# Kernel tuning notes

Hardware: AMD Instinct MI355X
Metric: run time of the kernel (lower is better)

The kernel has to match this reference:

```python
import jax, jax.numpy as jnp
import numpy as np

N = 50000      # nodes
E = 1600000    # edges
F_IN = 128     # input_dim
H = 160        # hidden_dim
G = 512        # graphs in batch
C = 2          # num_classes
EPS = 1e-5     # BatchNorm eps


def setup_inputs() -> dict:
    key = jax.random.key(0)
    ks = jax.random.split(key, 12)
    x = jax.random.normal(ks[0], (N, F_IN), jnp.float32)
    edge_index = jax.random.randint(ks[1], (2, E), 0, N, dtype=jnp.int32)
    batch = jnp.sort(jax.random.randint(ks[2], (N,), 0, G, dtype=jnp.int32))

    def lin(k, fi, fo):
        s = 1.0 / np.sqrt(fi)
        kw, kb = jax.random.split(k)
        W = jax.random.uniform(kw, (fi, fo), jnp.float32, -s, s)
        b = jax.random.uniform(kb, (fo,), jnp.float32, -s, s)
        return W, b

    W1, b1 = lin(ks[3], F_IN, H)
    W2, b2 = lin(ks[4], H, H)
    W3, b3 = lin(ks[5], H, H)
    Wc1, bc1 = lin(ks[6], H, H // 2)
    Wc2, bc2 = lin(ks[7], H // 2, C)

    def bn(k):
        k1, k2, k3, k4 = jax.random.split(k, 4)
        gamma = jax.random.uniform(k1, (H,), jnp.float32, 0.5, 1.5)
        beta = jax.random.normal(k2, (H,), jnp.float32) * 0.1
        mean = jax.random.normal(k3, (H,), jnp.float32) * 0.1
        var = jax.random.uniform(k4, (H,), jnp.float32, 0.5, 1.5)
        return gamma, beta, mean, var

    g1, be1, m1, v1 = bn(ks[8])
    g2, be2, m2, v2 = bn(ks[9])
    g3, be3, m3, v3 = bn(ks[10])

    return dict(x=x, edge_index=edge_index, batch=batch,
                W1=W1, b1=b1, W2=W2, b2=b2, W3=W3, b3=b3,
                g1=g1, be1=be1, m1=m1, v1=v1,
                g2=g2, be2=be2, m2=m2, v2=v2,
                g3=g3, be3=be3, m3=m3, v3=v3,
                Wc1=Wc1, bc1=bc1, Wc2=Wc2, bc2=bc2)


def gcn_conv(x, W, b, src, dst):
    """PyG GCNConv: symmetric deg normalization with self-loops; lin -> aggregate -> +bias."""
    n = x.shape[0]
    h = x @ W                                   # [N, H]
    loop = jnp.arange(n, dtype=src.dtype)
    s = jnp.concatenate([src, loop])            # self-loops appended
    d = jnp.concatenate([dst, loop])
    deg = jax.ops.segment_sum(jnp.ones_like(d, jnp.float32), d, num_segments=n)
    inv = jnp.where(deg > 0, jax.lax.rsqrt(deg), 0.0)
    msg = h[s] * (inv[s] * inv[d])[:, None]     # [E+N, H] gather + norm
    return jax.ops.segment_sum(msg, d, num_segments=n) + b


def bn_eval(x, gamma, beta, mean, var):
    return (x - mean) * jax.lax.rsqrt(var + EPS) * gamma + beta


def reference(x, edge_index, batch, W1, b1, W2, b2, W3, b3,
              g1, be1, m1, v1, g2, be2, m2, v2, g3, be3, m3, v3,
              Wc1, bc1, Wc2, bc2):
    src, dst = edge_index[0], edge_index[1]
    # eval mode: dropout is identity, BN uses running stats
    h = jax.nn.relu(bn_eval(gcn_conv(x, W1, b1, src, dst), g1, be1, m1, v1))
    h = jax.nn.relu(bn_eval(gcn_conv(h, W2, b2, src, dst), g2, be2, m2, v2))
    h = jax.nn.relu(bn_eval(gcn_conv(h, W3, b3, src, dst), g3, be3, m3, v3))
    # global mean pool over graph ids
    sums = jax.ops.segment_sum(h, batch, num_segments=G)
    cnt = jax.ops.segment_sum(jnp.ones((h.shape[0],), jnp.float32), batch, num_segments=G)
    pooled = sums / jnp.clip(cnt, 1.0)[:, None]
    # MLP head
    z = jax.nn.relu(pooled @ Wc1 + bc1)
    return z @ Wc2 + bc2
```

## Files before the change

kernel.cpp:

```cpp
#include <hip/hip_runtime.h>

#define N_NODES   50000
#define N_EDGES   1600000
#define FDIM_IN   128
#define HDIM      160
#define N_GRAPHS  512
#define BN_EPS    1e-5f
#define NBKT_MAX  256
#define BKT_SH    8
#define HIST_BLOCKS 128

typedef _Float16 h2   __attribute__((ext_vector_type(2)));
typedef _Float16 f16x8 __attribute__((ext_vector_type(8)));
typedef float  facc4 __attribute__((ext_vector_type(4)));


__device__ __forceinline__ unsigned short f2h_bits(float f) {
    union { _Float16 h; unsigned short s; } c;
    c.h = (_Float16)f;
    return c.s;
}

__device__ __forceinline__ unsigned int pkh(float lo, float hi) {
    return (unsigned int)f2h_bits(lo) | ((unsigned int)f2h_bits(hi) << 16);
}

__device__ __forceinline__ h2 u2h(unsigned int u) {
    union { unsigned int u; h2 h; } c; c.u = u; return c.h;
}

__device__ __forceinline__ unsigned int h2u(h2 h) {
    union { unsigned int u; h2 h; } c; c.h = h; return c.u;
}

__device__ __forceinline__ void addpk16(h2* acc, uint4 r) {
    acc[0] += u2h(r.x);
    acc[1] += u2h(r.y);
    acc[2] += u2h(r.z);
    acc[3] += u2h(r.w);
}


__global__ __launch_bounds__(256) void coarse_hist_kernel(const int* __restrict__ dst,
                                                          int* __restrict__ cg, int E) {
    __shared__ int h[NBKT_MAX];
    int tid = threadIdx.x;
    if (tid < NBKT_MAX) h[tid] = 0;
    __syncthreads();
    for (int e = blockIdx.x * 256 + tid; e < E; e += gridDim.x * 256)
        atomicAdd(&h[dst[e] >> BKT_SH], 1);
    __syncthreads();
    if (tid < NBKT_MAX) cg[blockIdx.x * NBKT_MAX + tid] = h[tid];
}


struct PrepArgs {
    const float *b, *g, *be, *m, *v;
    float *sc, *sh;
};

__global__ __launch_bounds__(256) void setup_kernel(const int* __restrict__ cg,
                                                    int* __restrict__ bucket_base,
                                                    int* __restrict__ bucket_cursor,
                                                    PrepArgs a0, PrepArgs a1, PrepArgs a2,
                                                    const float* __restrict__ W1,
                                                    const float* __restrict__ W2,
                                                    const float* __restrict__ W3,
                                                    unsigned short* __restrict__ o1,
                                                    unsigned short* __restrict__ o2,
                                                    unsigned short* __restrict__ o3) {
    int bid = blockIdx.x;
    int t = threadIdx.x;
    if (bid == 0) {
        __shared__ int h[NBKT_MAX];
        __shared__ int total;
        if (t < NBKT_MAX) {
            int s = 0;
            for (int b = 0; b < HIST_BLOCKS; ++b) s += cg[b * NBKT_MAX + t];
            h[t] = s;
        }
        __syncthreads();
        if (t == 0) {
            int run = 0;
            for (int i = 0; i < NBKT_MAX; ++i) { int c = h[i]; h[i] = run; run += c; }
            total = run;
        }
        __syncthreads();
        if (t < NBKT_MAX) {
            bucket_base[t] = h[t];
            bucket_cursor[t] = h[t];
        }
        if (t == 0) bucket_base[NBKT_MAX] = total;
    } else if (bid <= 3) {
        PrepArgs a = (bid == 1) ? a0 : (bid == 2) ? a1 : a2;
        if (t < HDIM) {
            float s = a.g[t] * rsqrtf(a.v[t] + BN_EPS);
            a.sc[t] = s;
            a.sh[t] = (a.b[t] - a.m[t]) * s + a.be[t];
        }
    } else {
        int i = (bid - 4) * 256 + t;
        const float* W;
        unsigned short* o;
        if (i < 128 * 160)                 { W = W1; o = o1; }
        else if (i < 128 * 160 + 160 * 160) { W = W2; o = o2; i -= 128 * 160; }
        else if (i < 128 * 160 + 2 * 160 * 160) { W = W3; o = o3; i -= 128 * 160 + 160 * 160; }
        else return;
        int j = i & 7;
        int l = (i >> 3) & 63;
        int u = (i >> 9) % 10;
        int tt = i / 5120;
        int k = tt * 32 + (l >> 4) * 8 + j;
        int nn = u * 16 + (l & 15);
        o[i] = f2h_bits(W[k * 160 + nn]);
    }
}

__global__ __launch_bounds__(256) void part_kernel(const int* __restrict__ src,
                                                   const int* __restrict__ dst,
                                                   int* __restrict__ bucket_cursor,
                                                   unsigned int* __restrict__ pairs, int E) {
    __shared__ int bcnt[NBKT_MAX], bbase[NBKT_MAX], lc[NBKT_MAX];
    int tid = threadIdx.x;
    int per = (E + gridDim.x - 1) / gridDim.x;
    int beg = blockIdx.x * per;
    int end = min(beg + per, E);
    if (tid < NBKT_MAX) { bcnt[tid] = 0; lc[tid] = 0; }
    __syncthreads();
    for (int e = beg + tid; e < end; e += 256)
        atomicAdd(&bcnt[dst[e] >> BKT_SH], 1);
    __syncthreads();
    if (tid < NBKT_MAX)
        bbase[tid] = bcnt[tid] ? atomicAdd(&bucket_cursor[tid], bcnt[tid]) : 0;
    __syncthreads();
    for (int e = beg + tid; e < end; e += 256) {
        int d = dst[e];
        int b = d >> BKT_SH;
        int pos = bbase[b] + atomicAdd(&lc[b], 1);
        pairs[pos] = ((unsigned int)src[e] << BKT_SH) | (unsigned int)(d & (NBKT_MAX - 1));
    }
}

__global__ __launch_bounds__(1024) void bucket_csr_kernel(const unsigned int* __restrict__ pairs,
                                                          const int* __restrict__ bucket_base,
                                                          int* __restrict__ row_off,
                                                          float* __restrict__ inv,
                                                          int* __restrict__ ssrc,
                                                          const float* __restrict__ x,
                                                          unsigned short* __restrict__ xs,
                                                          int n) {
    __shared__ int h[NBKT_MAX];
    __shared__ int ws[4];
    __shared__ float sinv[NBKT_MAX];
    int tid = threadIdx.x;
    int b = blockIdx.x;
    int node0 = b << BKT_SH;
    int beg = bucket_base[b], end = bucket_base[b + 1];
    if (tid < NBKT_MAX) h[tid] = 0;
    __syncthreads();
    for (int j = beg + tid; j < end; j += 1024)
        atomicAdd(&h[pairs[j] & (NBKT_MAX - 1)], 1);
    __syncthreads();
    int cntv = (tid < NBKT_MAX) ? h[tid] : 0;
    __syncthreads();
    int lane = tid & 63, wid = tid >> 6;
    int incl = cntv;
    #pragma unroll
    for (int off = 1; off < 64; off <<= 1) {
        int u = __shfl_up(incl, off);
        if (lane >= off) incl += u;
    }
    if (tid < NBKT_MAX && lane == 63) ws[wid] = incl;
    __syncthreads();
    if (tid == 0) {
        int r = 0;
        #pragma unroll
        for (int i = 0; i < 4; ++i) { int t = ws[i]; ws[i] = r; r += t; }
    }
    __syncthreads();
    int excl = (tid < NBKT_MAX) ? (ws[wid] + incl - cntv) : 0;
    if (tid < NBKT_MAX) {
        float iv = rsqrtf((float)(cntv + 1));
        int node = node0 + tid;
        if (node < n) {
            row_off[node] = beg + excl;
            inv[node] = iv;
        }
        sinv[tid] = iv;
        h[tid] = excl;
    }
    if (tid == 0 && (node0 + NBKT_MAX) >= n) row_off[n] = end;
    __syncthreads();
    for (int j = beg + tid; j < end; j += 1024) {
        unsigned int p = pairs[j];
        int pos = beg + atomicAdd(&h[p & (NBKT_MAX - 1)], 1);
        ssrc[pos] = (int)(p >> BKT_SH);
    }
    for (int idx = tid; idx < NBKT_MAX * 32; idx += 1024) {
        int nd = node0 + (idx >> 5);
        if (nd < n) {
            float w = sinv[idx >> 5];
            float4 v = ((const float4*)x)[(size_t)nd * 32 + (idx & 31)];
            ushort4 o;
            o.x = f2h_bits(v.x * w); o.y = f2h_bits(v.y * w);
            o.z = f2h_bits(v.z * w); o.w = f2h_bits(v.w * w);
            ((ushort4*)xs)[(size_t)nd * 32 + (idx & 31)] = o;
        }
    }
}


template <int CIN, int OUTMODE>
__global__ __launch_bounds__(64) void fused_layer_kernel(const unsigned short* __restrict__ in_s,
                                                         const float* __restrict__ inv,
                                                         const int* __restrict__ row_off,
                                                         const int* __restrict__ ssrc,
                                                         const unsigned short* __restrict__ Bp,
                                                         const float* __restrict__ sc,
                                                         const float* __restrict__ sh,
                                                         float* __restrict__ CoutF,
                                                         unsigned short* __restrict__ CoutB,
                                                         int n) {
    constexpr int LPR = CIN / 8;
    constexpr int G   = 64 / LPR;
    constexpr int RB  = CIN * 2;
    constexpr int KT  = CIN / 32;
    constexpr int STR = CIN + 8;
    __shared__ unsigned short hrow[16][STR];

    int lane = threadIdx.x;
    int node0 = blockIdx.x * 16;
    int g  = lane / LPR;
    int cl = lane - g * LPR;
    bool act = g < G;
    int lb = cl * 16;
    const char* bptr = (const char*)in_s;

    for (int i = 0; i < 16; ++i) {
        int node = node0 + i;
        if (node >= n) break;
        int beg = row_off[node], end = row_off[node + 1];

        h2 acc[4];
        #pragma unroll
        for (int k = 0; k < 4; ++k) acc[k] = (h2){(_Float16)0.f, (_Float16)0.f};

        if (g == 0) {
            uint4 r = *(const uint4*)(bptr + (size_t)node * RB + lb);
            addpk16(acc, r);
        }

        int e = act ? beg + g : end;
        for (; e + 3 * G < end; e += 4 * G) {
            int s0 = ssrc[e],         s1 = ssrc[e + G];
            int s2 = ssrc[e + 2 * G], s3 = ssrc[e + 3 * G];
            uint4 r0 = *(const uint4*)(bptr + (size_t)s0 * RB + lb);
            uint4 r1 = *(const uint4*)(bptr + (size_t)s1 * RB + lb);
            uint4 r2 = *(const uint4*)(bptr + (size_t)s2 * RB + lb);
            uint4 r3 = *(const uint4*)(bptr + (size_t)s3 * RB + lb);
            addpk16(acc, r0); addpk16(acc, r1);
            addpk16(acc, r2); addpk16(acc, r3);
        }
        if (e + G < end) {
            int s0 = ssrc[e], s1 = ssrc[e + G];
            uint4 r0 = *(const uint4*)(bptr + (size_t)s0 * RB + lb);
            uint4 r1 = *(const uint4*)(bptr + (size_t)s1 * RB + lb);
            addpk16(acc, r0); addpk16(acc, r1);
            e += 2 * G;
        }
        if (e < end) {
            uint4 r = *(const uint4*)(bptr + (size_t)ssrc[e] * RB + lb);
            addpk16(acc, r);
        }

        if (G == 4) {
            #pragma unroll
            for (int k = 0; k < 4; ++k) acc[k] += u2h(__shfl(h2u(acc[k]), lane + 32));
            #pragma unroll
            for (int k = 0; k < 4; ++k) acc[k] += u2h(__shfl(h2u(acc[k]), lane + 16));
        } else {
            #pragma unroll
            for (int k = 0; k < 4; ++k) {
                unsigned int ua = __shfl(h2u(acc[k]), lane + 20);
                unsigned int ub = __shfl(h2u(acc[k]), lane + 40);
                acc[k] += u2h(ua) + u2h(ub);
            }
        }

        if (lane < LPR) {
            float wi = inv[node];
            uint4 o;
            o.x = pkh((float)acc[0].x * wi, (float)acc[0].y * wi);
            o.y = pkh((float)acc[1].x * wi, (float)acc[1].y * wi);
            o.z = pkh((float)acc[2].x * wi, (float)acc[2].y * wi);
            o.w = pkh((float)acc[3].x * wi, (float)acc[3].y * wi);
            *(uint4*)&hrow[i][cl * 8] = o;
        }
    }
    __syncthreads();

    int m = lane & 15, q = lane >> 4;
    const f16x8* Bf = (const f16x8*)Bp;

    facc4 acc[10];
    #pragma unroll
    for (int u = 0; u < 10; ++u) acc[u] = (facc4){0.f, 0.f, 0.f, 0.f};

    #pragma unroll
    for (int t = 0; t < KT; ++t) {
        f16x8 af = *(const f16x8*)&hrow[m][t * 32 + q * 8];
        #pragma unroll
        for (int u = 0; u < 10; ++u) {
            f16x8 bf = Bf[(t * 10 + u) * 64 + lane];
            acc[u] = __builtin_amdgcn_mfma_f32_16x16x32_f16(af, bf, acc[u], 0, 0, 0);
        }
    }

    #pragma unroll
    for (int u = 0; u < 10; ++u) {
        int c = u * 16 + m;
        float scv = sc[c], shv = sh[c];
        #pragma unroll
        for (int r = 0; r < 4; ++r) {
            int rr = node0 + q * 4 + r;
            if (rr < n) {
                float v = fmaxf(acc[u][r] * scv + shv, 0.f);
                if (OUTMODE == 1) CoutB[(size_t)rr * 160 + c] = f2h_bits(v * inv[rr]);
                else              CoutF[(size_t)rr * 160 + c] = v;
            }
        }
    }
}


__global__ __launch_bounds__(256) void pool_head_kernel(const float* __restrict__ h,
                                                        const int* __restrict__ batch,
                                                        const float* __restrict__ Wc1,
                                                        const float* __restrict__ bc1,
                                                        const float* __restrict__ Wc2,
                                                        const float* __restrict__ bc2,
                                                        float* __restrict__ out, int n) {
    __shared__ float4 part[6][40];
    __shared__ float pooled[160];
    __shared__ float z[80];
    __shared__ int range[2];
    int g = blockIdx.x;
    int t = threadIdx.x;
    if (t < 2) {
        int target = g + t;
        int lo = 0, hi = n;
        while (lo < hi) {
            int mid = (lo + hi) >> 1;
            if (batch[mid] < target) lo = mid + 1; else hi = mid;
        }
        range[t] = lo;
    }
    __syncthreads();
    int lo = range[0], hi = range[1];
    int sub = t / 40, c4 = t - sub * 40;
    if (sub < 6) {
        float4 a = {0.f, 0.f, 0.f, 0.f};
        for (int r = lo + sub; r < hi; r += 6) {
            float4 v = ((const float4*)(h + (size_t)r * 160))[c4];
            a.x += v.x; a.y += v.y; a.z += v.z; a.w += v.w;
        }
        part[sub][c4] = a;
    }
    __syncthreads();
    if (t < 40) {
        float4 s = {0.f, 0.f, 0.f, 0.f};
        #pragma unroll
        for (int i = 0; i < 6; ++i) {
            float4 p = part[i][t];
            s.x += p.x; s.y += p.y; s.z += p.z; s.w += p.w;
        }
        float ic = 1.f / fmaxf((float)(hi - lo), 1.f);
        pooled[t * 4 + 0] = s.x * ic;
        pooled[t * 4 + 1] = s.y * ic;
        pooled[t * 4 + 2] = s.z * ic;
        pooled[t * 4 + 3] = s.w * ic;
    }
    __syncthreads();
    if (t < 80) {
        float s = bc1[t];
        for (int k = 0; k < 160; ++k) s += pooled[k] * Wc1[k * 80 + t];
        z[t] = fmaxf(s, 0.f);
    }
    __syncthreads();
    if (t < 2) {
        float s = bc2[t];
        for (int k = 0; k < 80; ++k) s += z[k] * Wc2[k * 2 + t];
        out[g * 2 + t] = s;
    }
}


static inline size_t align256(size_t x) { return (x + 255) & ~(size_t)255; }

extern "C" void kernel_launch(void* const* d_in, const int* in_sizes, int n_in,
                              void* d_out, int out_size, void* d_ws, size_t ws_size,
                              hipStream_t stream) {
    const float* x   = (const float*)d_in[0];
    const int* ei    = (const int*)d_in[1];
    const int* batch = (const int*)d_in[2];
    const float* W1  = (const float*)d_in[3];
    const float* b1  = (const float*)d_in[4];
    const float* W2  = (const float*)d_in[5];
    const float* b2  = (const float*)d_in[6];
    const float* W3  = (const float*)d_in[7];
    const float* b3  = (const float*)d_in[8];
    const float* g1  = (const float*)d_in[9];
    const float* be1 = (const float*)d_in[10];
    const float* m1  = (const float*)d_in[11];
    const float* v1  = (const float*)d_in[12];
    const float* g2  = (const float*)d_in[13];
    const float* be2 = (const float*)d_in[14];
    const float* m2  = (const float*)d_in[15];
    const float* v2  = (const float*)d_in[16];
    const float* g3  = (const float*)d_in[17];
    const float* be3 = (const float*)d_in[18];
    const float* m3  = (const float*)d_in[19];
    const float* v3  = (const float*)d_in[20];
    const float* Wc1 = (const float*)d_in[21];
    const float* bc1 = (const float*)d_in[22];
    const float* Wc2 = (const float*)d_in[23];
    const float* bc2 = (const float*)d_in[24];
    float* out = (float*)d_out;

    const int N = in_sizes[2];
    const int E = in_sizes[1] / 2;
    const int* src = ei;
    const int* dst = ei + E;

    char* w = (char*)d_ws;
    int*   row_off = (int*)w;             w += align256((size_t)(N + 1) * 4);
    float* inv     = (float*)w;           w += align256((size_t)N * 4);
    int*   ssrc    = (int*)w;             w += align256((size_t)E * 4);
    unsigned int* pairs = (unsigned int*)w; w += align256((size_t)E * 4);
    int*   cg      = (int*)w;             w += align256((size_t)HIST_BLOCKS * NBKT_MAX * 4);
    int*   bucket_base   = (int*)w;       w += align256((size_t)(NBKT_MAX + 1) * 4);
    int*   bucket_cursor = (int*)w;       w += align256((size_t)NBKT_MAX * 4);
    float* scsh    = (float*)w;           w += align256((size_t)6 * HDIM * 4);
    unsigned short* W1p = (unsigned short*)w;  w += align256((size_t)FDIM_IN * HDIM * 2);
    unsigned short* W2p = (unsigned short*)w;  w += align256((size_t)HDIM * HDIM * 2);
    unsigned short* W3p = (unsigned short*)w;  w += align256((size_t)HDIM * HDIM * 2);
    unsigned short* xs_bf  = (unsigned short*)w;  w += align256((size_t)N * FDIM_IN * 2);
    unsigned short* h1_bf  = (unsigned short*)w;  w += align256((size_t)N * HDIM * 2);
    unsigned short* h2_bf  = (unsigned short*)w;  w += align256((size_t)N * HDIM * 2);
    float* bufC    = (float*)w;           w += align256((size_t)N * HDIM * 4);
    float* sc1 = scsh, *sh1 = scsh + 160, *sc2 = scsh + 320, *sh2 = scsh + 480,
         * sc3 = scsh + 640, *sh3 = scsh + 800;

    coarse_hist_kernel<<<HIST_BLOCKS, 256, 0, stream>>>(dst, cg, E);

    PrepArgs pa0 = {b1, g1, be1, m1, v1, sc1, sh1};
    PrepArgs pa1 = {b2, g2, be2, m2, v2, sc2, sh2};
    PrepArgs pa2 = {b3, g3, be3, m3, v3, sc3, sh3};
    int packTotal = 128 * 160 + 2 * 160 * 160;
    int setupBlocks = 4 + (packTotal + 255) / 256;
    setup_kernel<<<setupBlocks, 256, 0, stream>>>(cg, bucket_base, bucket_cursor,
                                                  pa0, pa1, pa2, W1, W2, W3, W1p, W2p, W3p);

    part_kernel<<<256, 256, 0, stream>>>(src, dst, bucket_cursor, pairs, E);
    int nbkt = (N + NBKT_MAX - 1) >> BKT_SH;
    bucket_csr_kernel<<<nbkt, 1024, 0, stream>>>(pairs, bucket_base, row_off, inv, ssrc, x, xs_bf, N);

    int gF = (N + 15) / 16;

    fused_layer_kernel<128, 1><<<gF, 64, 0, stream>>>(xs_bf, inv, row_off, ssrc, W1p, sc1, sh1, nullptr, h1_bf, N);
    fused_layer_kernel<160, 1><<<gF, 64, 0, stream>>>(h1_bf, inv, row_off, ssrc, W2p, sc2, sh2, nullptr, h2_bf, N);
    fused_layer_kernel<160, 0><<<gF, 64, 0, stream>>>(h2_bf, inv, row_off, ssrc, W3p, sc3, sh3, bufC, nullptr, N);

    pool_head_kernel<<<N_GRAPHS, 256, 0, stream>>>(bufC, batch, Wc1, bc1, Wc2, bc2, out, N);
}
```

Before: 427.5 us.

## Split fused layer block across four waves for gather rows and MFMA tiles

Each 16-node block now runs with 256 threads: each of four wavefronts aggregates 4 of the 16 rows, and the MFMA output column tiles are distributed across waves instead of one wave computing all 10. The gather loop unroll is reduced from 4 to 2 neighbors per step, and out-of-range rows are zero-filled in shared memory. This aims to increase memory-level parallelism and latency hiding in the gather-bound phase, at the cost of fewer outstanding loads per wave and idle waves in the MFMA phase (10 tiles over 4 waves).

```diff
diff --git a/kernel.cpp b/kernel.cpp
--- a/kernel.cpp
+++ b/kernel.cpp
@@ -211,16 +211,16 @@
 
 
 template <int CIN, int OUTMODE>
-__global__ __launch_bounds__(64) void fused_layer_kernel(const unsigned short* __restrict__ in_s,
-                                                         const float* __restrict__ inv,
-                                                         const int* __restrict__ row_off,
-                                                         const int* __restrict__ ssrc,
-                                                         const unsigned short* __restrict__ Bp,
-                                                         const float* __restrict__ sc,
-                                                         const float* __restrict__ sh,
-                                                         float* __restrict__ CoutF,
-                                                         unsigned short* __restrict__ CoutB,
-                                                         int n) {
+__global__ __launch_bounds__(256) void fused_layer_kernel(const unsigned short* __restrict__ in_s,
+                                                          const float* __restrict__ inv,
+                                                          const int* __restrict__ row_off,
+                                                          const int* __restrict__ ssrc,
+                                                          const unsigned short* __restrict__ Bp,
+                                                          const float* __restrict__ sc,
+                                                          const float* __restrict__ sh,
+                                                          float* __restrict__ CoutF,
+                                                          unsigned short* __restrict__ CoutB,
+                                                          int n) {
     constexpr int LPR = CIN / 8;
     constexpr int G   = 64 / LPR;
     constexpr int RB  = CIN * 2;
@@ -228,7 +228,9 @@
     constexpr int STR = CIN + 8;
     __shared__ unsigned short hrow[16][STR];
 
-    int lane = threadIdx.x;
+    int tid  = threadIdx.x;
+    int wv   = tid >> 6;
+    int lane = tid & 63;
     int node0 = blockIdx.x * 16;
     int g  = lane / LPR;
     int cl = lane - g * LPR;
@@ -236,9 +238,16 @@
     int lb = cl * 16;
     const char* bptr = (const char*)in_s;
 
-    for (int i = 0; i < 16; ++i) {
-        int node = node0 + i;
-        if (node >= n) break;
+    for (int i = 0; i < 4; ++i) {
+        int row = wv * 4 + i;
+        int node = node0 + row;
+        if (node >= n) {
+            if (lane < LPR) {
+                uint4 z = {0u, 0u, 0u, 0u};
+                *(uint4*)&hrow[row][cl * 8] = z;
+            }
+            continue;
+        }
         int beg = row_off[node], end = row_off[node + 1];
 
         h2 acc[4];
@@ -251,22 +260,12 @@
         }
 
         int e = act ? beg + g : end;
-        for (; e + 3 * G < end; e += 4 * G) {
-            int s0 = ssrc[e],         s1 = ssrc[e + G];
-            int s2 = ssrc[e + 2 * G], s3 = ssrc[e + 3 * G];
-            uint4 r0 = *(const uint4*)(bptr + (size_t)s0 * RB + lb);
-            uint4 r1 = *(const uint4*)(bptr + (size_t)s1 * RB + lb);
-            uint4 r2 = *(const uint4*)(bptr + (size_t)s2 * RB + lb);
-            uint4 r3 = *(const uint4*)(bptr + (size_t)s3 * RB + lb);
-            addpk16(acc, r0); addpk16(acc, r1);
-            addpk16(acc, r2); addpk16(acc, r3);
-        }
-        if (e + G < end) {
+        for (; e + G < end; e += 2 * G) {
             int s0 = ssrc[e], s1 = ssrc[e + G];
             uint4 r0 = *(const uint4*)(bptr + (size_t)s0 * RB + lb);
             uint4 r1 = *(const uint4*)(bptr + (size_t)s1 * RB + lb);
-            addpk16(acc, r0); addpk16(acc, r1);
-            e += 2 * G;
+            addpk16(acc, r0);
+            addpk16(acc, r1);
         }
         if (e < end) {
             uint4 r = *(const uint4*)(bptr + (size_t)ssrc[e] * RB + lb);
@@ -294,7 +293,7 @@
             o.y = pkh((float)acc[1].x * wi, (float)acc[1].y * wi);
             o.z = pkh((float)acc[2].x * wi, (float)acc[2].y * wi);
             o.w = pkh((float)acc[3].x * wi, (float)acc[3].y * wi);
-            *(uint4*)&hrow[i][cl * 8] = o;
+            *(uint4*)&hrow[row][cl * 8] = o;
         }
     }
     __syncthreads();
@@ -302,29 +301,24 @@
     int m = lane & 15, q = lane >> 4;
     const f16x8* Bf = (const f16x8*)Bp;
 
-    facc4 acc[10];
+    f16x8 afr[KT];
     #pragma unroll
-    for (int u = 0; u < 10; ++u) acc[u] = (facc4){0.f, 0.f, 0.f, 0.f};
-
-    #pragma unroll
-    for (int t = 0; t < KT; ++t) {
-        f16x8 af = *(const f16x8*)&hrow[m][t * 32 + q * 8];
+    for (int t = 0; t < KT; ++t) afr[t] = *(const f16x8*)&hrow[m][t * 32 + q * 8];
+
+    for (int u = wv; u < 10; u += 4) {
+        facc4 acc = (facc4){0.f, 0.f, 0.f, 0.f};
         #pragma unroll
-        for (int u = 0; u < 10; ++u) {
+        for (int t = 0; t < KT; ++t) {
             f16x8 bf = Bf[(t * 10 + u) * 64 + lane];
-            acc[u] = __builtin_amdgcn_mfma_f32_16x16x32_f16(af, bf, acc[u], 0, 0, 0);
-        }
-    }
-
-    #pragma unroll
-    for (int u = 0; u < 10; ++u) {
+            acc = __builtin_amdgcn_mfma_f32_16x16x32_f16(afr[t], bf, acc, 0, 0, 0);
+        }
         int c = u * 16 + m;
         float scv = sc[c], shv = sh[c];
         #pragma unroll
         for (int r = 0; r < 4; ++r) {
             int rr = node0 + q * 4 + r;
             if (rr < n) {
-                float v = fmaxf(acc[u][r] * scv + shv, 0.f);
+                float v = fmaxf(acc[r] * scv + shv, 0.f);
                 if (OUTMODE == 1) CoutB[(size_t)rr * 160 + c] = f2h_bits(v * inv[rr]);
                 else              CoutF[(size_t)rr * 160 + c] = v;
             }
@@ -467,9 +461,9 @@
 
     int gF = (N + 15) / 16;
 
-    fused_layer_kernel<128, 1><<<gF, 64, 0, stream>>>(xs_bf, inv, row_off, ssrc, W1p, sc1, sh1, nullptr, h1_bf, N);
-    fused_layer_kernel<160, 1><<<gF, 64, 0, stream>>>(h1_bf, inv, row_off, ssrc, W2p, sc2, sh2, nullptr, h2_bf, N);
-    fused_layer_kernel<160, 0><<<gF, 64, 0, stream>>>(h2_bf, inv, row_off, ssrc, W3p, sc3, sh3, bufC, nullptr, N);
+    fused_layer_kernel<128, 1><<<gF, 256, 0, stream>>>(xs_bf, inv, row_off, ssrc, W1p, sc1, sh1, nullptr, h1_bf, N);
+    fused_layer_kernel<160, 1><<<gF, 256, 0, stream>>>(h1_bf, inv, row_off, ssrc, W2p, sc2, sh2, nullptr, h2_bf, N);
+    fused_layer_kernel<160, 0><<<gF, 256, 0, stream>>>(h2_bf, inv, row_off, ssrc, W3p, sc3, sh3, bufC, nullptr, N);
 
     pool_head_kernel<<<N_GRAPHS, 256, 0, stream>>>(bufC, batch, Wc1, bc1, Wc2, bc2, out, N);
 }
```

Measured after the change: 418.3 us. -2.2%, faster.
